# Performance work log

Measured on AMD Instinct MI355X. Metric: run time of the kernel, lower is better.

Reference implementation:

```python
import jax, jax.numpy as jnp
import numpy as np

B, T, N, D, H, L = 8, 200, 512, 4, 64, 32


def setup_inputs() -> dict:
    key = jax.random.key(0)
    ks = jax.random.split(key, 7)
    s = 1.0 / np.sqrt(H)  # torch GRU/Linear default init scale
    x = jax.random.normal(ks[0], (B, T, N, D), dtype=jnp.float32)
    W_ih = jax.random.uniform(ks[1], (3 * H, D), minval=-s, maxval=s, dtype=jnp.float32)
    W_hh = jax.random.uniform(ks[2], (3 * H, H), minval=-s, maxval=s, dtype=jnp.float32)
    b_ih = jax.random.uniform(ks[3], (3 * H,), minval=-s, maxval=s, dtype=jnp.float32)
    b_hh = jax.random.uniform(ks[4], (3 * H,), minval=-s, maxval=s, dtype=jnp.float32)
    W_enc = jax.random.uniform(ks[5], (L, H), minval=-s, maxval=s, dtype=jnp.float32)
    b_enc = jax.random.uniform(ks[6], (L,), minval=-s, maxval=s, dtype=jnp.float32)
    return {"trajectories": x, "W_ih": W_ih, "W_hh": W_hh, "b_ih": b_ih,
            "b_hh": b_hh, "W_enc": W_enc, "b_enc": b_enc}


def _gru_last_hidden(x, W_ih, W_hh, b_ih, b_hh):
    # x: [M, T, D] -> last hidden [M, H]; PyTorch GRU gate order (r, z, n)
    gx = jnp.einsum('mtd,gd->mtg', x, W_ih) + b_ih  # [M, T, 3H], input gates precomputed

    def step(h, gxt):
        gh = h @ W_hh.T + b_hh                      # [M, 3H]
        rz = jax.nn.sigmoid(gxt[:, :2 * H] + gh[:, :2 * H])
        r, z = rz[:, :H], rz[:, H:]
        n = jnp.tanh(gxt[:, 2 * H:] + r * gh[:, 2 * H:])
        h = (1.0 - z) * n + z * h
        return h, None

    h0 = jnp.zeros((x.shape[0], H), dtype=x.dtype)
    hT, _ = jax.lax.scan(step, h0, jnp.swapaxes(gx, 0, 1))  # scan over T
    return hT


def reference(trajectories, W_ih, W_hh, b_ih, b_hh, W_enc, b_enc):
    b, t, n, d = trajectories.shape
    # permute(1,0,2) per clip == move object axis before time, flatten all trajectories
    x = jnp.transpose(trajectories, (0, 2, 1, 3)).reshape(b * n, t, d)  # [M, T, D]
    hT = _gru_last_hidden(x, W_ih, W_hh, b_ih, b_hh)                    # [M, H]
    out = hT @ W_enc.T + b_enc                                          # [M, L]
    return out.reshape(b, n, L)  # list of [N, L] per clip, stacked
```

## Files before the change

kernel.cpp:

```cpp
#include <hip/hip_runtime.h>

#define TT 200
#define NN 512
#define DD 4
#define HH 64
#define LL 32
#define SB 8
#define BPB (NN / SB)
#define KP 72
#define LOG2E 1.44269504088896340736f

typedef short bf16x8 __attribute__((ext_vector_type(8)));
typedef float f32x4 __attribute__((ext_vector_type(4)));

union U8 { unsigned short s[8]; unsigned u[4]; bf16x8 v; };

__device__ __forceinline__ unsigned short hi16(float x) {
    return (unsigned short)(__float_as_uint(x) >> 16);
}

__global__ __launch_bounds__(256, 2)
void gru_traj_kernel(const float* __restrict__ xg,
                     const float* __restrict__ W_ih,
                     const float* __restrict__ W_hh,
                     const float* __restrict__ b_ih,
                     const float* __restrict__ b_hh,
                     const float* __restrict__ W_enc,
                     const float* __restrict__ b_enc,
                     float* __restrict__ out)
{
    __shared__ __align__(16) unsigned short hhi[2][SB][KP];
    __shared__ __align__(16) float hsf[SB][HH + 4];

    const int tid = threadIdx.x;
    const int bid = blockIdx.x;
    const int b   = bid >> 6;
    const int n0  = (bid & (BPB - 1)) * SB;

    const int w  = tid >> 6;
    const int l  = tid & 63;
    const int lr = l & 15;
    const int lg = l >> 4;
    const int s  = l & 7;
    const int hi8 = (lr >> 3) & 1;
    const int u0 = 16 * w + lg * 4;
    const int ub = u0 + 2 * hi8;

    const float sc[3] = { LOG2E, LOG2E, 2.0f * LOG2E };

    bf16x8 awh[3][2];
    #pragma unroll
    for (int i = 0; i < 3; ++i) {
        const int g = i * 64 + 16 * w + lr;
        #pragma unroll
        for (int kc = 0; kc < 2; ++kc) {
            const float* p = W_hh + g * HH + kc * 32 + lg * 8;
            U8 uh;
            #pragma unroll
            for (int j = 0; j < 8; ++j) uh.s[j] = hi16(p[j] * sc[i]);
            awh[i][kc] = uh.v;
        }
    }
    float wihc[3][2][4], cbrz[2][2], cbx[2], cbh[2];
    #pragma unroll
    for (int i = 0; i < 3; ++i) {
        #pragma unroll
        for (int k = 0; k < 2; ++k) {
            const int g = i * 64 + ub + k;
            #pragma unroll
            for (int d = 0; d < 4; ++d) wihc[i][k][d] = W_ih[g * DD + d] * sc[i];
            if (i < 2) cbrz[i][k] = (b_ih[g] + b_hh[g]) * sc[i];
            else       { cbx[k] = b_ih[g] * sc[2]; cbh[k] = b_hh[g] * sc[2]; }
        }
    }

    for (int idx = tid; idx < 2 * SB * KP / 2; idx += 256)
        reinterpret_cast<unsigned*>(hhi)[idx] = 0u;
    float hreg[2] = {0.f, 0.f};

    float4 xc = *reinterpret_cast<const float4*>(
        xg + ((size_t)(b * TT) * NN + n0 + s) * DD);
    __syncthreads();

    const bool hi8b = (hi8 != 0);
    const f32x4 z4 = {0.f, 0.f, 0.f, 0.f};

    #pragma unroll 2
    for (int t = 0; t < TT; ++t) {
        const int cur = t & 1, nxt = cur ^ 1;
        const int tn  = (t + 1 < TT) ? t + 1 : t;

        float4 xn = *reinterpret_cast<const float4*>(
            xg + ((size_t)(b * TT + tn) * NN + n0 + s) * DD);

        bf16x8 bh0 = *reinterpret_cast<const bf16x8*>(&hhi[cur][s][lg * 8]);
        bf16x8 bh1 = *reinterpret_cast<const bf16x8*>(&hhi[cur][s][32 + lg * 8]);

        float gxv[3][2];
        #pragma unroll
        for (int i = 0; i < 3; ++i) {
            #pragma unroll
            for (int k = 0; k < 2; ++k) {
                const float c0 = (i < 2) ? cbrz[i][k] : cbx[k];
                gxv[i][k] = fmaf(wihc[i][k][0], xc.x, fmaf(wihc[i][k][1], xc.y,
                            fmaf(wihc[i][k][2], xc.z, fmaf(wihc[i][k][3], xc.w, c0))));
            }
        }

        f32x4 aR = __builtin_amdgcn_mfma_f32_16x16x32_bf16(awh[0][0], bh0, z4, 0,0,0);
        f32x4 aZ = __builtin_amdgcn_mfma_f32_16x16x32_bf16(awh[1][0], bh0, z4, 0,0,0);
        f32x4 aN = __builtin_amdgcn_mfma_f32_16x16x32_bf16(awh[2][0], bh0, z4, 0,0,0);
        aR = __builtin_amdgcn_mfma_f32_16x16x32_bf16(awh[0][1], bh1, aR, 0,0,0);
        aZ = __builtin_amdgcn_mfma_f32_16x16x32_bf16(awh[1][1], bh1, aZ, 0,0,0);
        aN = __builtin_amdgcn_mfma_f32_16x16x32_bf16(awh[2][1], bh1, aN, 0,0,0);

        float vR0 = hi8b ? aR[2] : aR[0];
        float vR1 = hi8b ? aR[3] : aR[1];
        float vZ0 = hi8b ? aZ[2] : aZ[0];
        float vZ1 = hi8b ? aZ[3] : aZ[1];
        float vN0 = hi8b ? aN[2] : aN[0];
        float vN1 = hi8b ? aN[3] : aN[1];

        float hn0, hn1;
        {
            float sR  = vR0 + gxv[0][0];
            float sZ  = vZ0 + gxv[1][0];
            float ghn = vN0 + cbh[0];
            float rg = __builtin_amdgcn_rcpf(1.0f + __builtin_amdgcn_exp2f(-sR));
            float ez = __builtin_amdgcn_exp2f(-sZ);
            float na = fmaf(rg, ghn, gxv[2][0]);
            float e  = __builtin_amdgcn_exp2f(-na);
            float nn = fmaf(2.0f, __builtin_amdgcn_rcpf(1.0f + e), -1.0f);
            float z  = __builtin_amdgcn_rcpf(1.0f + ez);
            hn0 = fmaf(z, hreg[0] - nn, nn);
            hreg[0] = hn0;
        }
        {
            float sR  = vR1 + gxv[0][1];
            float sZ  = vZ1 + gxv[1][1];
            float ghn = vN1 + cbh[1];
            float rg = __builtin_amdgcn_rcpf(1.0f + __builtin_amdgcn_exp2f(-sR));
            float ez = __builtin_amdgcn_exp2f(-sZ);
            float na = fmaf(rg, ghn, gxv[2][1]);
            float e  = __builtin_amdgcn_exp2f(-na);
            float nn = fmaf(2.0f, __builtin_amdgcn_rcpf(1.0f + e), -1.0f);
            float z  = __builtin_amdgcn_rcpf(1.0f + ez);
            hn1 = fmaf(z, hreg[1] - nn, nn);
            hreg[1] = hn1;
        }

        unsigned ph = __builtin_amdgcn_perm(__float_as_uint(hn1), __float_as_uint(hn0),
                                            0x07060302u);
        *reinterpret_cast<unsigned*>(&hhi[nxt][s][ub]) = ph;
        xc = xn;
        __syncthreads();
    }

    hsf[s][ub]     = hreg[0];
    hsf[s][ub + 1] = hreg[1];
    __syncthreads();
    {
        const int so = tid >> 5, li = tid & 31;
        float a = b_enc[li];
        #pragma unroll
        for (int k = 0; k < HH; ++k)
            a = fmaf(hsf[so][k], W_enc[li * HH + k], a);
        out[(bid * SB + so) * LL + li] = a;
    }
}

extern "C" void kernel_launch(void* const* d_in, const int* in_sizes, int n_in,
                              void* d_out, int out_size, void* d_ws, size_t ws_size,
                              hipStream_t stream) {
    const float* xg    = (const float*)d_in[0];
    const float* W_ih  = (const float*)d_in[1];
    const float* W_hh  = (const float*)d_in[2];
    const float* b_ih  = (const float*)d_in[3];
    const float* b_hh  = (const float*)d_in[4];
    const float* W_enc = (const float*)d_in[5];
    const float* b_enc = (const float*)d_in[6];
    float* out = (float*)d_out;

    dim3 grid(8 * BPB), block(256);
    hipLaunchKernelGGL(gru_traj_kernel, grid, block, 0, stream,
                       xg, W_ih, W_hh, b_ih, b_hh, W_enc, b_enc, out);
}
```

Baseline: 92.21 us.

## Halve sequences per block to double grid size and per-thread gate work

Each block now handles 4 trajectories instead of 8, so the grid doubles to 1024 blocks and occupancy bounds rise to 4 blocks per CU. Each lane now computes one hidden unit for one sequence instead of two, which shortens the serial per-step elementwise chain. The MFMA still runs on a 16-wide column tile, so only 4 of its 16 columns are useful and the hardware does the same matrix work per block. More blocks give more latency hiding across the 200 serial steps, at the cost of more total MFMA and barrier work overall.

```diff
diff --git a/kernel.cpp b/kernel.cpp
--- a/kernel.cpp
+++ b/kernel.cpp
@@ -5,7 +5,7 @@
 #define DD 4
 #define HH 64
 #define LL 32
-#define SB 8
+#define SB 4
 #define BPB (NN / SB)
 #define KP 72
 #define LOG2E 1.44269504088896340736f
@@ -19,7 +19,7 @@
     return (unsigned short)(__float_as_uint(x) >> 16);
 }
 
-__global__ __launch_bounds__(256, 2)
+__global__ __launch_bounds__(256, 4)
 void gru_traj_kernel(const float* __restrict__ xg,
                      const float* __restrict__ W_ih,
                      const float* __restrict__ W_hh,
@@ -34,17 +34,16 @@
 
     const int tid = threadIdx.x;
     const int bid = blockIdx.x;
-    const int b   = bid >> 6;
+    const int b   = bid >> 7;
     const int n0  = (bid & (BPB - 1)) * SB;
 
     const int w  = tid >> 6;
     const int l  = tid & 63;
     const int lr = l & 15;
     const int lg = l >> 4;
-    const int s  = l & 7;
-    const int hi8 = (lr >> 3) & 1;
-    const int u0 = 16 * w + lg * 4;
-    const int ub = u0 + 2 * hi8;
+    const int s  = lr & 3;
+    const int rq = (lr >> 2) & 3;
+    const int uo = 16 * w + lg * 4 + rq;
 
     const float sc[3] = { LOG2E, LOG2E, 2.0f * LOG2E };
 
@@ -61,28 +60,28 @@
             awh[i][kc] = uh.v;
         }
     }
-    float wihc[3][2][4], cbrz[2][2], cbx[2], cbh[2];
+    float wihc[3][4], cb0, cb1, cbx, cbh;
     #pragma unroll
     for (int i = 0; i < 3; ++i) {
+        const int g = i * 64 + uo;
         #pragma unroll
-        for (int k = 0; k < 2; ++k) {
-            const int g = i * 64 + ub + k;
-            #pragma unroll
-            for (int d = 0; d < 4; ++d) wihc[i][k][d] = W_ih[g * DD + d] * sc[i];
-            if (i < 2) cbrz[i][k] = (b_ih[g] + b_hh[g]) * sc[i];
-            else       { cbx[k] = b_ih[g] * sc[2]; cbh[k] = b_hh[g] * sc[2]; }
-        }
+        for (int d = 0; d < 4; ++d) wihc[i][d] = W_ih[g * DD + d] * sc[i];
     }
+    cb0 = (b_ih[uo] + b_hh[uo]) * sc[0];
+    cb1 = (b_ih[64 + uo] + b_hh[64 + uo]) * sc[1];
+    cbx = b_ih[128 + uo] * sc[2];
+    cbh = b_hh[128 + uo] * sc[2];
 
     for (int idx = tid; idx < 2 * SB * KP / 2; idx += 256)
         reinterpret_cast<unsigned*>(hhi)[idx] = 0u;
-    float hreg[2] = {0.f, 0.f};
+    float hreg = 0.f;
 
     float4 xc = *reinterpret_cast<const float4*>(
         xg + ((size_t)(b * TT) * NN + n0 + s) * DD);
     __syncthreads();
 
-    const bool hi8b = (hi8 != 0);
+    const bool selb0 = ((rq & 1) != 0);
+    const bool selb1 = ((rq & 2) != 0);
     const f32x4 z4 = {0.f, 0.f, 0.f, 0.f};
 
     #pragma unroll 2
@@ -96,16 +95,12 @@
         bf16x8 bh0 = *reinterpret_cast<const bf16x8*>(&hhi[cur][s][lg * 8]);
         bf16x8 bh1 = *reinterpret_cast<const bf16x8*>(&hhi[cur][s][32 + lg * 8]);
 
-        float gxv[3][2];
-        #pragma unroll
-        for (int i = 0; i < 3; ++i) {
-            #pragma unroll
-            for (int k = 0; k < 2; ++k) {
-                const float c0 = (i < 2) ? cbrz[i][k] : cbx[k];
-                gxv[i][k] = fmaf(wihc[i][k][0], xc.x, fmaf(wihc[i][k][1], xc.y,
-                            fmaf(wihc[i][k][2], xc.z, fmaf(wihc[i][k][3], xc.w, c0))));
-            }
-        }
+        float gxr = fmaf(wihc[0][0], xc.x, fmaf(wihc[0][1], xc.y,
+                    fmaf(wihc[0][2], xc.z, fmaf(wihc[0][3], xc.w, cb0))));
+        float gxz = fmaf(wihc[1][0], xc.x, fmaf(wihc[1][1], xc.y,
+                    fmaf(wihc[1][2], xc.z, fmaf(wihc[1][3], xc.w, cb1))));
+        float gxn = fmaf(wihc[2][0], xc.x, fmaf(wihc[2][1], xc.y,
+                    fmaf(wihc[2][2], xc.z, fmaf(wihc[2][3], xc.w, cbx))));
 
         f32x4 aR = __builtin_amdgcn_mfma_f32_16x16x32_bf16(awh[0][0], bh0, z4, 0,0,0);
         f32x4 aZ = __builtin_amdgcn_mfma_f32_16x16x32_bf16(awh[1][0], bh0, z4, 0,0,0);
@@ -114,52 +109,36 @@
         aZ = __builtin_amdgcn_mfma_f32_16x16x32_bf16(awh[1][1], bh1, aZ, 0,0,0);
         aN = __builtin_amdgcn_mfma_f32_16x16x32_bf16(awh[2][1], bh1, aN, 0,0,0);
 
-        float vR0 = hi8b ? aR[2] : aR[0];
-        float vR1 = hi8b ? aR[3] : aR[1];
-        float vZ0 = hi8b ? aZ[2] : aZ[0];
-        float vZ1 = hi8b ? aZ[3] : aZ[1];
-        float vN0 = hi8b ? aN[2] : aN[0];
-        float vN1 = hi8b ? aN[3] : aN[1];
+        float vR01 = selb0 ? aR[1] : aR[0];
+        float vR23 = selb0 ? aR[3] : aR[2];
+        float vR   = selb1 ? vR23 : vR01;
+        float vZ01 = selb0 ? aZ[1] : aZ[0];
+        float vZ23 = selb0 ? aZ[3] : aZ[2];
+        float vZ   = selb1 ? vZ23 : vZ01;
+        float vN01 = selb0 ? aN[1] : aN[0];
+        float vN23 = selb0 ? aN[3] : aN[2];
+        float vN   = selb1 ? vN23 : vN01;
 
-        float hn0, hn1;
-        {
-            float sR  = vR0 + gxv[0][0];
-            float sZ  = vZ0 + gxv[1][0];
-            float ghn = vN0 + cbh[0];
-            float rg = __builtin_amdgcn_rcpf(1.0f + __builtin_amdgcn_exp2f(-sR));
-            float ez = __builtin_amdgcn_exp2f(-sZ);
-            float na = fmaf(rg, ghn, gxv[2][0]);
-            float e  = __builtin_amdgcn_exp2f(-na);
-            float nn = fmaf(2.0f, __builtin_amdgcn_rcpf(1.0f + e), -1.0f);
-            float z  = __builtin_amdgcn_rcpf(1.0f + ez);
-            hn0 = fmaf(z, hreg[0] - nn, nn);
-            hreg[0] = hn0;
-        }
-        {
-            float sR  = vR1 + gxv[0][1];
-            float sZ  = vZ1 + gxv[1][1];
-            float ghn = vN1 + cbh[1];
-            float rg = __builtin_amdgcn_rcpf(1.0f + __builtin_amdgcn_exp2f(-sR));
-            float ez = __builtin_amdgcn_exp2f(-sZ);
-            float na = fmaf(rg, ghn, gxv[2][1]);
-            float e  = __builtin_amdgcn_exp2f(-na);
-            float nn = fmaf(2.0f, __builtin_amdgcn_rcpf(1.0f + e), -1.0f);
-            float z  = __builtin_amdgcn_rcpf(1.0f + ez);
-            hn1 = fmaf(z, hreg[1] - nn, nn);
-            hreg[1] = hn1;
-        }
+        float sR  = vR + gxr;
+        float sZ  = vZ + gxz;
+        float ghn = vN + cbh;
+        float rg = __builtin_amdgcn_rcpf(1.0f + __builtin_amdgcn_exp2f(-sR));
+        float ez = __builtin_amdgcn_exp2f(-sZ);
+        float na = fmaf(rg, ghn, gxn);
+        float e  = __builtin_amdgcn_exp2f(-na);
+        float nn = fmaf(2.0f, __builtin_amdgcn_rcpf(1.0f + e), -1.0f);
+        float z  = __builtin_amdgcn_rcpf(1.0f + ez);
+        float hn = fmaf(z, hreg - nn, nn);
+        hreg = hn;
 
-        unsigned ph = __builtin_amdgcn_perm(__float_as_uint(hn1), __float_as_uint(hn0),
-                                            0x07060302u);
-        *reinterpret_cast<unsigned*>(&hhi[nxt][s][ub]) = ph;
+        hhi[nxt][s][uo] = hi16(hn);
         xc = xn;
         __syncthreads();
     }
 
-    hsf[s][ub]     = hreg[0];
-    hsf[s][ub + 1] = hreg[1];
+    hsf[s][uo] = hreg;
     __syncthreads();
-    {
+    if (tid < SB * LL) {
         const int so = tid >> 5, li = tid & 31;
         float a = b_enc[li];
         #pragma unroll
```

Measured after the change: 105.1 us. +14.0%, slower.
